# Kernel tuning notes

Hardware: AMD Instinct MI355X
Metric: run time of the kernel (lower is better)

Reference implementation:

```python
import jax, jax.numpy as jnp
import numpy as np

N_NODES = 100000
N_EDGES = 3200000


def _gat_conv(x, src, dst, ea, Wx, We, a_src, a_dst, a_edge, b, n):
    # PyG GATConv, heads=1, edge_dim set: h = x@Wx^T, he = ea@We^T
    h = x @ Wx.T                      # [N,16]
    he = ea @ We.T                    # [E,16]
    alpha = h[src] @ a_src + h[dst] @ a_dst + he @ a_edge  # [E]
    alpha = jnp.where(alpha > 0, alpha, 0.2 * alpha)       # leaky_relu(0.2)
    m = jax.ops.segment_max(alpha, dst, num_segments=n)
    m = jnp.where(jnp.isfinite(m), m, 0.0)
    ex = jnp.exp(alpha - m[dst])
    s = jax.ops.segment_sum(ex, dst, num_segments=n)
    a = ex / (s[dst] + 1e-16)
    out = jax.ops.segment_sum(a[:, None] * h[src], dst, num_segments=n)
    return out + b


def setup_inputs() -> dict:
    key = jax.random.key(0)
    ks = iter(jax.random.split(key, 40))
    rn = lambda shape, s=0.1: jax.random.normal(next(ks), shape, dtype=jnp.float32) * s
    inp = {}
    inp['x'] = jax.random.normal(next(ks), (N_NODES, 4), dtype=jnp.float32)
    inp['edge_index'] = jax.random.randint(next(ks), (2, N_EDGES), 0, N_NODES, dtype=jnp.int64)
    inp['edge_attr'] = jax.random.normal(next(ks), (N_EDGES, 6), dtype=jnp.float32)
    # conv1: GATConv(4->16, edge_dim=6)
    inp['c1_Wx'] = rn((16, 4)); inp['c1_We'] = rn((16, 6))
    inp['c1_asrc'] = rn((16,)); inp['c1_adst'] = rn((16,)); inp['c1_aedge'] = rn((16,))
    inp['c1_b'] = rn((16,))
    # edge1 MLP: 38->32->64->32->16
    inp['e1_w1'] = rn((32, 38)); inp['e1_b1'] = rn((32,))
    inp['e1_w2'] = rn((64, 32)); inp['e1_b2'] = rn((64,))
    inp['e1_w3'] = rn((32, 64)); inp['e1_b3'] = rn((32,))
    inp['e1_w4'] = rn((16, 32)); inp['e1_b4'] = rn((16,))
    # conv2: GATConv(16->16, edge_dim=16)
    inp['c2_Wx'] = rn((16, 16)); inp['c2_We'] = rn((16, 16))
    inp['c2_asrc'] = rn((16,)); inp['c2_adst'] = rn((16,)); inp['c2_aedge'] = rn((16,))
    inp['c2_b'] = rn((16,))
    # node head 16->16->2, edge head 16->16->4
    inp['nl_w1'] = rn((16, 16)); inp['nl_b1'] = rn((16,))
    inp['nl_w2'] = rn((2, 16)); inp['nl_b2'] = rn((2,))
    inp['el_w1'] = rn((16, 16)); inp['el_b1'] = rn((16,))
    inp['el_w2'] = rn((4, 16)); inp['el_b2'] = rn((4,))
    return inp


def reference(x, edge_index, edge_attr,
              c1_Wx, c1_We, c1_asrc, c1_adst, c1_aedge, c1_b,
              e1_w1, e1_b1, e1_w2, e1_b2, e1_w3, e1_b3, e1_w4, e1_b4,
              c2_Wx, c2_We, c2_asrc, c2_adst, c2_aedge, c2_b,
              nl_w1, nl_b1, nl_w2, nl_b2,
              el_w1, el_b1, el_w2, el_b2):
    n = x.shape[0]
    src, dst = edge_index[0], edge_index[1]
    x1 = _gat_conv(x, src, dst, edge_attr, c1_Wx, c1_We, c1_asrc, c1_adst, c1_aedge, c1_b, n)
    # edge MLP on [x_src | edge_attr | x_dst] (dropout = identity in eval)
    e = jnp.concatenate([x1[src], edge_attr, x1[dst]], axis=1)  # [E,38]
    e = jax.nn.relu(e @ e1_w1.T + e1_b1)
    e = jax.nn.relu(e @ e1_w2.T + e1_b2)
    e = jax.nn.relu(e @ e1_w3.T + e1_b3)
    e = e @ e1_w4.T + e1_b4                                     # [E,16]
    x2 = _gat_conv(x1, src, dst, e, c2_Wx, c2_We, c2_asrc, c2_adst, c2_aedge, c2_b, n)
    node = jax.nn.relu(jax.nn.relu(x2 @ nl_w1.T + nl_b1) @ nl_w2.T + nl_b2)
    edge = jax.nn.relu(jax.nn.relu(e @ el_w1.T + el_b1) @ el_w2.T + el_b2)
    return (jax.nn.log_softmax(node, axis=1), jax.nn.log_softmax(edge, axis=1))
```

## Files before the change

kernel.cpp:

```cpp
#include <hip/hip_runtime.h>

#define NN 100000
#define NE 3200000
#define NB 98

typedef unsigned int u32;
typedef unsigned short u16;
typedef _Float16 f16x2 __attribute__((ext_vector_type(2)));
typedef __fp16 fp16v2 __attribute__((ext_vector_type(2)));

__device__ __forceinline__ int clampi(int s){
  s = s < 0 ? 0 : s;
  return s >= NN ? NN-1 : s;
}

__device__ __forceinline__ f16x2 pk2(float x, float y){
  fp16v2 r = __builtin_amdgcn_cvt_pkrtz(x, y);
  return __builtin_bit_cast(f16x2, r);
}
__device__ __forceinline__ float dot2(f16x2 a, f16x2 b, float c){
  return __builtin_amdgcn_fdot2(a, b, c, false);
}
__device__ __forceinline__ float f16lo(u32 w){
  __fp16 h = __builtin_bit_cast(__fp16, (u16)(w & 0xffffu));
  return (float)h;
}
__device__ __forceinline__ float f16hi(u32 w){
  __fp16 h = __builtin_bit_cast(__fp16, (u16)(w >> 16));
  return (float)h;
}
__device__ __forceinline__ float f16u(u16 w){
  __fp16 h = __builtin_bit_cast(__fp16, w);
  return (float)h;
}

__global__ __launch_bounds__(256,8) void khist(const int* __restrict__ ei, int* __restrict__ cnt){
  int i = blockIdx.x*256 + threadIdx.x;
  if (i >= NE) return;
  atomicAdd(&cnt[clampi(ei[NE+i])], 1);
}

__global__ __launch_bounds__(1024) void kscanA(const int* __restrict__ cnt, int* __restrict__ bsum){
  __shared__ int wsum[16];
  int tid = threadIdx.x;
  int i = blockIdx.x*1024 + tid;
  int x = (i < NN) ? cnt[i] : 0;
  #pragma unroll
  for (int ofs = 1; ofs < 64; ofs <<= 1) x += __shfl_xor(x, ofs, 64);
  if ((tid & 63) == 0) wsum[tid >> 6] = x;
  __syncthreads();
  if (tid == 0){
    int t = 0;
    #pragma unroll
    for (int k = 0; k < 16; k++) t += wsum[k];
    bsum[blockIdx.x] = t;
  }
}

__global__ void kscanB(const int* __restrict__ bsum, int* __restrict__ boff, int* __restrict__ offN){
  if (threadIdx.x == 0){
    int c = 0;
    for (int b = 0; b < NB; b++){ boff[b] = c; c += bsum[b]; }
    offN[0] = c;
  }
}

__global__ __launch_bounds__(1024) void kscanC(int* __restrict__ cnt, const int* __restrict__ boff,
                                               int* __restrict__ off){
  __shared__ int wsum[16];
  int tid = threadIdx.x;
  int i = blockIdx.x*1024 + tid;
  int v = (i < NN) ? cnt[i] : 0;
  int x = v;
  #pragma unroll
  for (int ofs = 1; ofs < 64; ofs <<= 1){
    int t = __shfl_up(x, ofs, 64);
    if ((tid & 63) >= ofs) x += t;
  }
  if ((tid & 63) == 63) wsum[tid >> 6] = x;
  __syncthreads();
  if (tid < 16){
    int y = wsum[tid];
    #pragma unroll
    for (int ofs = 1; ofs < 16; ofs <<= 1){
      int t = __shfl_up(y, ofs, 64);
      if (tid >= ofs) y += t;
    }
    wsum[tid] = y;
  }
  __syncthreads();
  int wb = (tid >= 64) ? wsum[(tid >> 6) - 1] : 0;
  if (i < NN){ off[i] = boff[blockIdx.x] + wb + x - v; cnt[i] = 0; }
}

__global__ __launch_bounds__(256,4) void k1(const float* __restrict__ x,
    const float* __restrict__ Wx, const float* __restrict__ asrc, const float* __restrict__ adst,
    float* __restrict__ hs1, float* __restrict__ hd1)
{
  __shared__ float wL[64], aS[16], aD[16];
  int tid = threadIdx.x;
  if (tid < 64) wL[tid] = Wx[tid];
  if (tid < 16){ aS[tid] = asrc[tid]; aD[tid] = adst[tid]; }
  __syncthreads();
  int n = blockIdx.x*256 + tid;
  if (n >= NN) return;
  float4 xr = ((const float4*)x)[n];
  float hs=0.f, hd=0.f;
  #pragma unroll
  for (int j=0;j<16;j++){
    float h = xr.x*wL[j*4+0] + xr.y*wL[j*4+1] + xr.z*wL[j*4+2] + xr.w*wL[j*4+3];
    hs += h*aS[j]; hd += h*aD[j];
  }
  hs1[n]=hs; hd1[n]=hd;
}

__global__ __launch_bounds__(256,8) void k2a(const int* __restrict__ ei,
    const float* __restrict__ ea, const float* __restrict__ We, const float* __restrict__ aedge,
    const float* __restrict__ hs1, const float* __restrict__ hd1,
    const int* __restrict__ off, int* __restrict__ cnt, float2* __restrict__ edata)
{
  __shared__ float w6[6];
  int tid = threadIdx.x;
  if (tid < 6){
    float acc = 0.f;
    for (int j=0;j<16;j++) acc += aedge[j] * We[j*6+tid];
    w6[tid] = acc;
  }
  __syncthreads();
  int i = blockIdx.x*256 + tid;
  if (i >= NE) return;
  int s = clampi(ei[i]);
  int d = clampi(ei[NE + i]);
  const float2* eap = (const float2*)ea + (size_t)i*3;
  float2 u0 = eap[0], u1 = eap[1], u2 = eap[2];
  float al = hs1[s] + hd1[d]
    + u0.x*w6[0] + u0.y*w6[1] + u1.x*w6[2]
    + u1.y*w6[3] + u2.x*w6[4] + u2.y*w6[5];
  al = al > 0.f ? al : 0.2f*al;
  float ex = __expf(al);
  int pos = off[d] + atomicAdd(&cnt[d], 1);
  edata[pos] = make_float2(ex, __int_as_float(s));
}

__global__ __launch_bounds__(256,8) void k34(const float2* __restrict__ edata,
    const int* __restrict__ off, const float* __restrict__ x,
    const float* __restrict__ c1b, const float* __restrict__ Wx1, const float* __restrict__ Wx2,
    const float* __restrict__ a2s, const float* __restrict__ a2d,
    const float* __restrict__ w1p,
    u32* __restrict__ hpk, float* __restrict__ hs2, float* __restrict__ hd2,
    u32* __restrict__ uh, u32* __restrict__ vh, int* __restrict__ cnt)
{
  __shared__ float w0L[64], bL[16], wL[256], aS[16], aD[16];
  __shared__ float w1sL[32*16], w1dL[32*16];
  int tid = threadIdx.x;
  wL[tid] = Wx2[tid];
  if (tid < 64) w0L[tid] = Wx1[tid];
  if (tid < 16){ bL[tid]=c1b[tid]; aS[tid]=a2s[tid]; aD[tid]=a2d[tid]; }
  for (int idx=tid; idx<512; idx+=256){
    int j=idx>>4, k=idx&15;
    w1sL[idx] = w1p[j*38+k];
    w1dL[idx] = w1p[j*38+22+k];
  }
  __syncthreads();
  int t = blockIdx.x*256 + tid;
  int n = t >> 4;
  int j = t & 15;
  if (n >= NN) return;
  int f = j & 3, ks = j >> 2;
  int beg = off[n], end = off[n+1];
  float aj = 0.f, sl = 0.f;
  for (int k = beg + ks; k < end; k += 4){
    float2 p = edata[k];
    int src = __float_as_int(p.y);
    aj += p.x * x[(size_t)src*4 + f];
    sl += p.x;
  }
  aj += __shfl_xor(aj, 4, 64); aj += __shfl_xor(aj, 8, 64);
  sl += __shfl_xor(sl, 4, 64); sl += __shfl_xor(sl, 8, 64);
  float inv = 1.f/(sl + 1e-16f);
  float m0 = __shfl(aj, 0, 16)*inv;
  float m1 = __shfl(aj, 1, 16)*inv;
  float m2 = __shfl(aj, 2, 16)*inv;
  float m3 = __shfl(aj, 3, 16)*inv;
  float xvj = m0*w0L[j*4+0] + m1*w0L[j*4+1] + m2*w0L[j*4+2] + m3*w0L[j*4+3] + bL[j];
  float hv = 0.f, u0=0.f, u1=0.f, v0=0.f, v1=0.f;
  #pragma unroll
  for (int k=0;k<16;k++){
    float vk = __shfl(xvj, k, 16);
    hv += vk * wL[j*16+k];
    u0 += vk * w1sL[(2*j)*16+k];
    u1 += vk * w1sL[(2*j+1)*16+k];
    v0 += vk * w1dL[(2*j)*16+k];
    v1 += vk * w1dL[(2*j+1)*16+k];
  }
  ((u16*)hpk)[(size_t)n*16 + j] = (u16)(__builtin_bit_cast(u32, pk2(hv, 0.f)) & 0xffffu);
  uh[(size_t)n*16 + j] = __builtin_bit_cast(u32, pk2(u0, u1));
  vh[(size_t)n*16 + j] = __builtin_bit_cast(u32, pk2(v0, v1));
  float hsp = hv*aS[j], hdp = hv*aD[j];
  #pragma unroll
  for (int ofs=1; ofs<16; ofs<<=1){
    hsp += __shfl_xor(hsp, ofs, 64);
    hdp += __shfl_xor(hdp, ofs, 64);
  }
  if (j == 0){ hs2[n]=hsp; hd2[n]=hdp; cnt[n]=0; }
}

__global__ __launch_bounds__(256,8) void k5(
    const int* __restrict__ ei, const float* __restrict__ ea,
    const u32* __restrict__ uh, const u32* __restrict__ vh,
    const float* __restrict__ hs2, const float* __restrict__ hd2,
    const float* w1p, const float* b1p, const float* w2p, const float* b2p,
    const float* w3p, const float* b3p, const float* w4p, const float* b4p,
    const float* We2, const float* a2e,
    const float* ew1p, const float* eb1p, const float* ew2p, const float* eb2p,
    const int* __restrict__ off, int* __restrict__ cnt, float2* __restrict__ edata,
    float* __restrict__ eout)
{
  __shared__ __align__(16) f16x2 w1eh[32*4];  __shared__ float b1L[32];
  __shared__ __align__(16) f16x2 w2h[64*16];  __shared__ float b2L[64];
  __shared__ __align__(16) f16x2 w3h[32*32];  __shared__ float b3L[32];
  __shared__ __align__(16) f16x2 w4h[16*16];  __shared__ float b4L[16];
  __shared__ __align__(16) f16x2 ew1h[16*8];  __shared__ float eb1L[16];
  __shared__ __align__(16) f16x2 ew2h[4*8];   __shared__ float eb2L[4];
  __shared__ __align__(16) f16x2 w16h[8];
  int tid = threadIdx.x;
  if (tid < 128){
    int j=tid>>2, kk=tid&3;
    int k0=2*kk, k1=2*kk+1;
    float v0 = (k0<6) ? w1p[j*38+16+k0] : 0.f;
    float v1 = (k1<6) ? w1p[j*38+16+k1] : 0.f;
    w1eh[tid] = pk2(v0, v1);
  }
  for (int idx=tid; idx<1024; idx+=256){
    int j=idx>>4, kk=idx&15;
    w2h[idx] = pk2(w2p[j*32+2*kk], w2p[j*32+2*kk+1]);
  }
  for (int idx=tid; idx<1024; idx+=256){
    int j=idx>>5, kk=idx&31;
    w3h[idx] = pk2(w3p[j*64+2*kk], w3p[j*64+2*kk+1]);
  }
  if (tid < 256){
    int j=tid>>4, kk=tid&15;
    w4h[tid] = pk2(w4p[j*32+2*kk], w4p[j*32+2*kk+1]);
  }
  if (tid < 128){
    int j=tid>>3, kk=tid&7;
    ew1h[tid] = pk2(ew1p[j*16+2*kk], ew1p[j*16+2*kk+1]);
  }
  if (tid < 32){
    int j=tid>>3, kk=tid&7;
    ew2h[tid] = pk2(ew2p[j*16+2*kk], ew2p[j*16+2*kk+1]);
  }
  if (tid < 8){
    float s0=0.f, s1=0.f;
    for (int j=0;j<16;j++){
      s0 += a2e[j] * We2[j*16 + 2*tid];
      s1 += a2e[j] * We2[j*16 + 2*tid + 1];
    }
    w16h[tid] = pk2(s0, s1);
  }
  if (tid < 64) b2L[tid] = b2p[tid];
  if (tid < 32){ b1L[tid] = b1p[tid]; b3L[tid] = b3p[tid]; }
  if (tid < 16){ b4L[tid] = b4p[tid]; eb1L[tid] = eb1p[tid]; }
  if (tid < 4)  eb2L[tid] = eb2p[tid];
  __syncthreads();

  int i = blockIdx.x*256 + tid;
  if (i >= NE) return;
  int s = clampi(ei[i]);
  int d = clampi(ei[NE + i]);

  f16x2 a1h[16];
  {
    const float2* eap = (const float2*)ea + (size_t)i*3;
    float2 e0=eap[0], e1=eap[1], e2=eap[2];
    f16x2 eh[4];
    eh[0]=pk2(e0.x,e0.y); eh[1]=pk2(e1.x,e1.y); eh[2]=pk2(e2.x,e2.y); eh[3]=pk2(0.f,0.f);
    const uint4* up = (const uint4*)(uh + (size_t)s*16);
    const uint4* vp = (const uint4*)(vh + (size_t)d*16);
    uint4 U[4], V[4];
    #pragma unroll
    for (int q=0;q<4;q++){ U[q]=up[q]; V[q]=vp[q]; }
    u32 uw[16], vw[16];
    #pragma unroll
    for (int q=0;q<4;q++){
      uw[4*q]=U[q].x; uw[4*q+1]=U[q].y; uw[4*q+2]=U[q].z; uw[4*q+3]=U[q].w;
      vw[4*q]=V[q].x; vw[4*q+1]=V[q].y; vw[4*q+2]=V[q].z; vw[4*q+3]=V[q].w;
    }
    #pragma unroll
    for (int j=0;j<16;j++){
      float t0 = b1L[2*j]   + f16lo(uw[j]) + f16lo(vw[j]);
      float t1 = b1L[2*j+1] + f16hi(uw[j]) + f16hi(vw[j]);
      #pragma unroll
      for (int kk=0;kk<4;kk++){
        t0 = dot2(eh[kk], w1eh[(2*j)*4+kk],   t0);
        t1 = dot2(eh[kk], w1eh[(2*j+1)*4+kk], t1);
      }
      a1h[j] = pk2(fmaxf(t0,0.f), fmaxf(t1,0.f));
    }
  }
  f16x2 a2h[32];
  #pragma unroll
  for (int j=0;j<32;j++){
    float acc0 = b2L[2*j], acc1 = b2L[2*j+1];
    #pragma unroll
    for (int kk=0;kk<16;kk++){
      acc0 = dot2(a1h[kk], w2h[(2*j)*16+kk],   acc0);
      acc1 = dot2(a1h[kk], w2h[(2*j+1)*16+kk], acc1);
    }
    a2h[j] = pk2(fmaxf(acc0,0.f), fmaxf(acc1,0.f));
  }
  f16x2 a3h[16];
  #pragma unroll
  for (int j=0;j<16;j++){
    float acc0 = b3L[2*j], acc1 = b3L[2*j+1];
    #pragma unroll
    for (int kk=0;kk<32;kk++){
      acc0 = dot2(a2h[kk], w3h[(2*j)*32+kk],   acc0);
      acc1 = dot2(a2h[kk], w3h[(2*j+1)*32+kk], acc1);
    }
    a3h[j] = pk2(fmaxf(acc0,0.f), fmaxf(acc1,0.f));
  }
  f16x2 eh4[8];
  #pragma unroll
  for (int j=0;j<8;j++){
    float acc0 = b4L[2*j], acc1 = b4L[2*j+1];
    #pragma unroll
    for (int kk=0;kk<16;kk++){
      acc0 = dot2(a3h[kk], w4h[(2*j)*16+kk],   acc0);
      acc1 = dot2(a3h[kk], w4h[(2*j+1)*16+kk], acc1);
    }
    eh4[j] = pk2(acc0, acc1);
  }
  f16x2 th[8];
  #pragma unroll
  for (int j=0;j<8;j++){
    float acc0 = eb1L[2*j], acc1 = eb1L[2*j+1];
    #pragma unroll
    for (int kk=0;kk<8;kk++){
      acc0 = dot2(eh4[kk], ew1h[(2*j)*8+kk],   acc0);
      acc1 = dot2(eh4[kk], ew1h[(2*j+1)*8+kk], acc1);
    }
    th[j] = pk2(fmaxf(acc0,0.f), fmaxf(acc1,0.f));
  }
  float y0 = eb2L[0], y1 = eb2L[1], y2 = eb2L[2], y3 = eb2L[3];
  #pragma unroll
  for (int kk=0;kk<8;kk++){
    y0 = dot2(th[kk], ew2h[0*8+kk], y0);
    y1 = dot2(th[kk], ew2h[1*8+kk], y1);
    y2 = dot2(th[kk], ew2h[2*8+kk], y2);
    y3 = dot2(th[kk], ew2h[3*8+kk], y3);
  }
  y0 = fmaxf(y0,0.f); y1 = fmaxf(y1,0.f); y2 = fmaxf(y2,0.f); y3 = fmaxf(y3,0.f);
  float m = fmaxf(fmaxf(y0,y1), fmaxf(y2,y3));
  float l = m + __logf(__expf(y0-m)+__expf(y1-m)+__expf(y2-m)+__expf(y3-m));
  float4 eo; eo.x = y0-l; eo.y = y1-l; eo.z = y2-l; eo.w = y3-l;
  ((float4*)eout)[i] = eo;

  float al = hs2[s] + hd2[d];
  #pragma unroll
  for (int kk=0;kk<8;kk++) al = dot2(eh4[kk], w16h[kk], al);
  al = al > 0.f ? al : 0.2f*al;
  float ex = __expf(al);
  int pos = off[d] + atomicAdd(&cnt[d], 1);
  edata[pos] = make_float2(ex, __int_as_float(s));
}

__global__ __launch_bounds__(256,8) void kagg2(const float2* __restrict__ edata,
    const int* __restrict__ off, const u16* __restrict__ hpk,
    const float* __restrict__ c2b,
    const float* __restrict__ w1p, const float* __restrict__ b1p,
    const float* __restrict__ w2p, const float* __restrict__ b2p,
    float* __restrict__ nout, int* __restrict__ cnt)
{
  __shared__ float w1L[256], cb[16], b1L[16], w2L[32], b2L[2];
  int tid = threadIdx.x;
  w1L[tid] = w1p[tid];
  if (tid < 16){ cb[tid] = c2b[tid]; b1L[tid] = b1p[tid]; }
  if (tid < 32) w2L[tid] = w2p[tid];
  if (tid < 2)  b2L[tid] = b2p[tid];
  __syncthreads();
  int t = blockIdx.x*256 + tid;
  int n = t >> 6;
  int l = t & 63;
  if (n >= NN) return;
  int j = l & 15, ks = l >> 4;
  int beg = off[n], end = off[n+1];
  float aj = 0.f, sl = 0.f;
  for (int k = beg + ks; k < end; k += 4){
    float2 p = edata[k];
    int src = __float_as_int(p.y);
    aj += p.x * f16u(hpk[(size_t)src*16 + j]);
    sl += p.x;
  }
  aj += __shfl_xor(aj, 16, 64); aj += __shfl_xor(aj, 32, 64);
  sl += __shfl_xor(sl, 16, 64); sl += __shfl_xor(sl, 32, 64);
  float inv = 1.f/(sl + 1e-16f);
  float vj = aj*inv + cb[j];
  float tj = b1L[j];
  #pragma unroll
  for (int k=0;k<16;k++){
    float vk = __shfl(vj, k, 16);
    tj += vk * w1L[j*16 + k];
  }
  tj = fmaxf(tj, 0.f);
  float p0 = tj * w2L[j];
  float p1 = tj * w2L[16 + j];
  #pragma unroll
  for (int ofs=1; ofs<16; ofs<<=1){
    p0 += __shfl_xor(p0, ofs, 64);
    p1 += __shfl_xor(p1, ofs, 64);
  }
  if (l == 0){
    float y0 = fmaxf(p0 + b2L[0], 0.f);
    float y1 = fmaxf(p1 + b2L[1], 0.f);
    float m = fmaxf(y0, y1);
    float lg = m + __logf(__expf(y0-m) + __expf(y1-m));
    float2 no; no.x = y0-lg; no.y = y1-lg;
    ((float2*)nout)[n] = no;
    cnt[n] = 0;
  }
}

extern "C" void kernel_launch(void* const* d_in, const int* in_sizes, int n_in,
                              void* d_out, int out_size, void* d_ws, size_t ws_size,
                              hipStream_t stream)
{
  const float* x  = (const float*)d_in[0];
  const int* ei   = (const int*)d_in[1];
  const float* ea = (const float*)d_in[2];
  const float* c1Wx = (const float*)d_in[3];
  const float* c1We = (const float*)d_in[4];
  const float* c1as = (const float*)d_in[5];
  const float* c1ad = (const float*)d_in[6];
  const float* c1ae = (const float*)d_in[7];
  const float* c1b  = (const float*)d_in[8];
  const float* e1w1 = (const float*)d_in[9];
  const float* e1b1 = (const float*)d_in[10];
  const float* e1w2 = (const float*)d_in[11];
  const float* e1b2 = (const float*)d_in[12];
  const float* e1w3 = (const float*)d_in[13];
  const float* e1b3 = (const float*)d_in[14];
  const float* e1w4 = (const float*)d_in[15];
  const float* e1b4 = (const float*)d_in[16];
  const float* c2Wx = (const float*)d_in[17];
  const float* c2We = (const float*)d_in[18];
  const float* c2as = (const float*)d_in[19];
  const float* c2ad = (const float*)d_in[20];
  const float* c2ae = (const float*)d_in[21];
  const float* c2b  = (const float*)d_in[22];
  const float* nlw1 = (const float*)d_in[23];
  const float* nlb1 = (const float*)d_in[24];
  const float* nlw2 = (const float*)d_in[25];
  const float* nlb2 = (const float*)d_in[26];
  const float* elw1 = (const float*)d_in[27];
  const float* elb1 = (const float*)d_in[28];
  const float* elw2 = (const float*)d_in[29];
  const float* elb2 = (const float*)d_in[30];

  float* ws = (float*)d_ws;
  const size_t N = NN;
  int* off   = (int*)ws;
  int* cnt   = (int*)ws + (N + 8);
  int* bsum  = (int*)ws + (2*N + 8);
  int* boff  = (int*)ws + (2*N + 136);
  u32* hpk   = (u32*)(ws + 2*N + 264);
  float* hs  = ws + 10*N + 264;
  float* hd  = hs + N;
  u32* uh    = (u32*)(hd + N);
  u32* vh    = uh + 16*N;
  float2* edata = (float2*)(vh + 16*N);

  float* nout = (float*)d_out;
  float* eout = (float*)d_out + 200000;

  const int GE = (NE + 255)/256;
  const int GN = (NN + 255)/256;

  (void)hipMemsetAsync(cnt, 0, N*sizeof(int), stream);
  khist<<<GE, 256, 0, stream>>>(ei, cnt);
  kscanA<<<NB, 1024, 0, stream>>>(cnt, bsum);
  kscanB<<<1, 64, 0, stream>>>(bsum, boff, off + NN);
  kscanC<<<NB, 1024, 0, stream>>>(cnt, boff, off);
  k1<<<GN, 256, 0, stream>>>(x, c1Wx, c1as, c1ad, hs, hd);
  k2a<<<GE, 256, 0, stream>>>(ei, ea, c1We, c1ae, hs, hd, off, cnt, edata);
  k34<<<(NN*16 + 255)/256, 256, 0, stream>>>(edata, off, x,
      c1b, c1Wx, c2Wx, c2as, c2ad, e1w1, hpk, hs, hd, uh, vh, cnt);
  k5<<<GE, 256, 0, stream>>>(ei, ea, uh, vh, hs, hd,
      e1w1, e1b1, e1w2, e1b2, e1w3, e1b3, e1w4, e1b4,
      c2We, c2ae, elw1, elb1, elw2, elb2,
      off, cnt, edata, eout);
  kagg2<<<(NN*64 + 255)/256, 256, 0, stream>>>(edata, off, (const u16*)hpk,
      c2b, nlw1, nlb1, nlw2, nlb2, nout, cnt);
}
```

Before: 766.7 us.

## Run edge MLP layers 2-3 on MFMA and fold layer 4 into downstream weights

The per-edge MLP's 32->64 and 64->32 layers move from per-thread fdot2 loops to 16x16x32 f16 MFMA instructions. Each wave stages its activations through shared memory in 16-row tiles. The linear fourth layer is folded algebraically into the edge-head first layer and into the attention-edge vector, which removes a matmul per edge. The costs are extra LDS traffic, many block-wide barriers inside the tile loop, and lower occupancy from launch bounds 4 and larger shared memory. The NE bounds check is dropped, which is safe only because NE is a multiple of 256.

```diff
diff --git a/kernel.cpp b/kernel.cpp
--- a/kernel.cpp
+++ b/kernel.cpp
@@ -7,6 +7,8 @@
 typedef unsigned int u32;
 typedef unsigned short u16;
 typedef _Float16 f16x2 __attribute__((ext_vector_type(2)));
+typedef _Float16 f16x8 __attribute__((ext_vector_type(8)));
+typedef float fltx4 __attribute__((ext_vector_type(4)));
 typedef __fp16 fp16v2 __attribute__((ext_vector_type(2)));
 
 __device__ __forceinline__ int clampi(int s){
@@ -17,6 +19,9 @@
 __device__ __forceinline__ f16x2 pk2(float x, float y){
   fp16v2 r = __builtin_amdgcn_cvt_pkrtz(x, y);
   return __builtin_bit_cast(f16x2, r);
+}
+__device__ __forceinline__ u32 pk2u(float x, float y){
+  return __builtin_bit_cast(u32, pk2(x, y));
 }
 __device__ __forceinline__ float dot2(f16x2 a, f16x2 b, float c){
   return __builtin_amdgcn_fdot2(a, b, c, false);
@@ -193,9 +198,9 @@
     v0 += vk * w1dL[(2*j)*16+k];
     v1 += vk * w1dL[(2*j+1)*16+k];
   }
-  ((u16*)hpk)[(size_t)n*16 + j] = (u16)(__builtin_bit_cast(u32, pk2(hv, 0.f)) & 0xffffu);
-  uh[(size_t)n*16 + j] = __builtin_bit_cast(u32, pk2(u0, u1));
-  vh[(size_t)n*16 + j] = __builtin_bit_cast(u32, pk2(v0, v1));
+  ((u16*)hpk)[(size_t)n*16 + j] = (u16)(pk2u(hv, 0.f) & 0xffffu);
+  uh[(size_t)n*16 + j] = pk2u(u0, u1);
+  vh[(size_t)n*16 + j] = pk2u(v0, v1);
   float hsp = hv*aS[j], hdp = hv*aD[j];
   #pragma unroll
   for (int ofs=1; ofs<16; ofs<<=1){
@@ -205,7 +210,7 @@
   if (j == 0){ hs2[n]=hsp; hd2[n]=hdp; cnt[n]=0; }
 }
 
-__global__ __launch_bounds__(256,8) void k5(
+__global__ __launch_bounds__(256,4) void k5m(
     const int* __restrict__ ei, const float* __restrict__ ea,
     const u32* __restrict__ uh, const u32* __restrict__ vh,
     const float* __restrict__ hs2, const float* __restrict__ hd2,
@@ -216,13 +221,17 @@
     const int* __restrict__ off, int* __restrict__ cnt, float2* __restrict__ edata,
     float* __restrict__ eout)
 {
+  __shared__ __align__(16) u32 a13L[4][1024];
+  __shared__ __align__(16) u32 a2L[4][512];
+  __shared__ __align__(16) uint4 b2f[4][64];
+  __shared__ __align__(16) uint4 b3f[4][64];
   __shared__ __align__(16) f16x2 w1eh[32*4];  __shared__ float b1L[32];
-  __shared__ __align__(16) f16x2 w2h[64*16];  __shared__ float b2L[64];
-  __shared__ __align__(16) f16x2 w3h[32*32];  __shared__ float b3L[32];
-  __shared__ __align__(16) f16x2 w4h[16*16];  __shared__ float b4L[16];
-  __shared__ __align__(16) f16x2 ew1h[16*8];  __shared__ float eb1L[16];
+  __shared__ float b2L[64], b3L[32];
+  __shared__ __align__(16) f16x2 M1h[16*16];  __shared__ float c1L[16];
   __shared__ __align__(16) f16x2 ew2h[4*8];   __shared__ float eb2L[4];
-  __shared__ __align__(16) f16x2 w16h[8];
+  __shared__ __align__(16) f16x2 w16w4h[16];
+  __shared__ float w16L[16];  __shared__ float w16b4L;
+
   int tid = threadIdx.x;
   if (tid < 128){
     int j=tid>>2, kk=tid&3;
@@ -231,46 +240,75 @@
     float v1 = (k1<6) ? w1p[j*38+16+k1] : 0.f;
     w1eh[tid] = pk2(v0, v1);
   }
-  for (int idx=tid; idx<1024; idx+=256){
-    int j=idx>>4, kk=idx&15;
-    w2h[idx] = pk2(w2p[j*32+2*kk], w2p[j*32+2*kk+1]);
-  }
-  for (int idx=tid; idx<1024; idx+=256){
-    int j=idx>>5, kk=idx&31;
-    w3h[idx] = pk2(w3p[j*64+2*kk], w3p[j*64+2*kk+1]);
-  }
-  if (tid < 256){
-    int j=tid>>4, kk=tid&15;
-    w4h[tid] = pk2(w4p[j*32+2*kk], w4p[j*32+2*kk+1]);
-  }
-  if (tid < 128){
-    int j=tid>>3, kk=tid&7;
-    ew1h[tid] = pk2(ew1p[j*16+2*kk], ew1p[j*16+2*kk+1]);
+  {
+    int c = tid>>6, l = tid&63;
+    int j = c*16 + (l&15), kb = (l>>4)*8;
+    const float* src = w2p + j*32 + kb;
+    uint4 q;
+    q.x = pk2u(src[0], src[1]); q.y = pk2u(src[2], src[3]);
+    q.z = pk2u(src[4], src[5]); q.w = pk2u(src[6], src[7]);
+    b2f[c][l] = q;
+  }
+  {
+    int kt = tid>>7, c = (tid>>6)&1, l = tid&63;
+    int j = c*16 + (l&15), kb = kt*32 + (l>>4)*8;
+    const float* src = w3p + j*64 + kb;
+    uint4 q;
+    q.x = pk2u(src[0], src[1]); q.y = pk2u(src[2], src[3]);
+    q.z = pk2u(src[4], src[5]); q.w = pk2u(src[6], src[7]);
+    b3f[kt*2+c][l] = q;
+  }
+  if (tid < 64) b2L[tid] = b2p[tid];
+  if (tid < 32){ b1L[tid] = b1p[tid]; b3L[tid] = b3p[tid]; }
+  {
+    int o = tid>>4, p = tid&15;
+    float m0=0.f, m1=0.f;
+    #pragma unroll
+    for (int q=0;q<16;q++){
+      float w = ew1p[o*16+q];
+      m0 += w * w4p[q*32 + 2*p];
+      m1 += w * w4p[q*32 + 2*p + 1];
+    }
+    M1h[o*16+p] = pk2(m0, m1);
+  }
+  if (tid < 16){
+    float acc = eb1p[tid];
+    for (int q=0;q<16;q++) acc += ew1p[tid*16+q]*b4p[q];
+    c1L[tid] = acc;
+    float w=0.f;
+    for (int j=0;j<16;j++) w += a2e[j] * We2[j*16+tid];
+    w16L[tid] = w;
   }
   if (tid < 32){
     int j=tid>>3, kk=tid&7;
     ew2h[tid] = pk2(ew2p[j*16+2*kk], ew2p[j*16+2*kk+1]);
   }
-  if (tid < 8){
+  if (tid < 4) eb2L[tid] = eb2p[tid];
+  __syncthreads();
+  if (tid < 16){
     float s0=0.f, s1=0.f;
-    for (int j=0;j<16;j++){
-      s0 += a2e[j] * We2[j*16 + 2*tid];
-      s1 += a2e[j] * We2[j*16 + 2*tid + 1];
-    }
-    w16h[tid] = pk2(s0, s1);
-  }
-  if (tid < 64) b2L[tid] = b2p[tid];
-  if (tid < 32){ b1L[tid] = b1p[tid]; b3L[tid] = b3p[tid]; }
-  if (tid < 16){ b4L[tid] = b4p[tid]; eb1L[tid] = eb1p[tid]; }
-  if (tid < 4)  eb2L[tid] = eb2p[tid];
-  __syncthreads();
-
+    for (int q=0;q<16;q++){
+      s0 += w16L[q]*w4p[q*32 + 2*tid];
+      s1 += w16L[q]*w4p[q*32 + 2*tid + 1];
+    }
+    w16w4h[tid] = pk2(s0, s1);
+  }
+  if (tid == 0){
+    float acc=0.f;
+    for (int q=0;q<16;q++) acc += w16L[q]*b4p[q];
+    w16b4L = acc;
+  }
+  __syncthreads();
+
+  int wid = tid>>6, lane = tid&63;
+  int cl = lane & 15, g = lane >> 4;
+  u32* a13 = a13L[wid];
+  u32* a2u = a2L[wid];
   int i = blockIdx.x*256 + tid;
-  if (i >= NE) return;
   int s = clampi(ei[i]);
   int d = clampi(ei[NE + i]);
 
-  f16x2 a1h[16];
+  u32 a1h[16];
   {
     const float2* eap = (const float2*)ea + (size_t)i*3;
     float2 e0=eap[0], e1=eap[1], e2=eap[2];
@@ -296,52 +334,82 @@
         t0 = dot2(eh[kk], w1eh[(2*j)*4+kk],   t0);
         t1 = dot2(eh[kk], w1eh[(2*j+1)*4+kk], t1);
       }
-      a1h[j] = pk2(fmaxf(t0,0.f), fmaxf(t1,0.f));
-    }
-  }
-  f16x2 a2h[32];
-  #pragma unroll
-  for (int j=0;j<32;j++){
-    float acc0 = b2L[2*j], acc1 = b2L[2*j+1];
-    #pragma unroll
-    for (int kk=0;kk<16;kk++){
-      acc0 = dot2(a1h[kk], w2h[(2*j)*16+kk],   acc0);
-      acc1 = dot2(a1h[kk], w2h[(2*j+1)*16+kk], acc1);
-    }
-    a2h[j] = pk2(fmaxf(acc0,0.f), fmaxf(acc1,0.f));
-  }
-  f16x2 a3h[16];
-  #pragma unroll
-  for (int j=0;j<16;j++){
-    float acc0 = b3L[2*j], acc1 = b3L[2*j+1];
-    #pragma unroll
-    for (int kk=0;kk<32;kk++){
-      acc0 = dot2(a2h[kk], w3h[(2*j)*32+kk],   acc0);
-      acc1 = dot2(a2h[kk], w3h[(2*j+1)*32+kk], acc1);
-    }
-    a3h[j] = pk2(fmaxf(acc0,0.f), fmaxf(acc1,0.f));
-  }
-  f16x2 eh4[8];
-  #pragma unroll
-  for (int j=0;j<8;j++){
-    float acc0 = b4L[2*j], acc1 = b4L[2*j+1];
-    #pragma unroll
-    for (int kk=0;kk<16;kk++){
-      acc0 = dot2(a3h[kk], w4h[(2*j)*16+kk],   acc0);
-      acc1 = dot2(a3h[kk], w4h[(2*j+1)*16+kk], acc1);
-    }
-    eh4[j] = pk2(acc0, acc1);
+      a1h[j] = pk2u(fmaxf(t0,0.f), fmaxf(t1,0.f));
+    }
+  }
+  {
+    uint4* dst = (uint4*)(a13 + lane*16);
+    dst[0] = make_uint4(a1h[0],a1h[1],a1h[2],a1h[3]);
+    dst[1] = make_uint4(a1h[4],a1h[5],a1h[6],a1h[7]);
+    dst[2] = make_uint4(a1h[8],a1h[9],a1h[10],a1h[11]);
+    dst[3] = make_uint4(a1h[12],a1h[13],a1h[14],a1h[15]);
+  }
+  f16x8 fb2[4], fb3[4];
+  #pragma unroll
+  for (int c=0;c<4;c++) fb2[c] = __builtin_bit_cast(f16x8, b2f[c][lane]);
+  #pragma unroll
+  for (int q=0;q<4;q++) fb3[q] = __builtin_bit_cast(f16x8, b3f[q][lane]);
+  __syncthreads();
+
+  #pragma unroll
+  for (int r=0;r<4;r++){
+    __syncthreads();
+    uint4 av = *(const uint4*)(a13 + (r*16 + cl)*16 + g*4);
+    f16x8 af = __builtin_bit_cast(f16x8, av);
+    _Float16* a2h_ = (_Float16*)a2u;
+    #pragma unroll
+    for (int c=0;c<4;c++){
+      float b = b2L[c*16 + cl];
+      fltx4 acc = {b,b,b,b};
+      acc = __builtin_amdgcn_mfma_f32_16x16x32_f16(af, fb2[c], acc, 0, 0, 0);
+      int col = c*16 + cl;
+      int rowb = g*4;
+      a2h_[(rowb+0)*64 + col] = (_Float16)fmaxf(acc[0], 0.f);
+      a2h_[(rowb+1)*64 + col] = (_Float16)fmaxf(acc[1], 0.f);
+      a2h_[(rowb+2)*64 + col] = (_Float16)fmaxf(acc[2], 0.f);
+      a2h_[(rowb+3)*64 + col] = (_Float16)fmaxf(acc[3], 0.f);
+    }
+    __syncthreads();
+    uint4 a20 = *(const uint4*)(a2u + cl*32 + g*4);
+    uint4 a21 = *(const uint4*)(a2u + cl*32 + 16 + g*4);
+    f16x8 af0 = __builtin_bit_cast(f16x8, a20);
+    f16x8 af1 = __builtin_bit_cast(f16x8, a21);
+    _Float16* a3w = (_Float16*)a13;
+    #pragma unroll
+    for (int c=0;c<2;c++){
+      float b = b3L[c*16 + cl];
+      fltx4 acc = {b,b,b,b};
+      acc = __builtin_amdgcn_mfma_f32_16x16x32_f16(af0, fb3[0*2+c], acc, 0, 0, 0);
+      acc = __builtin_amdgcn_mfma_f32_16x16x32_f16(af1, fb3[1*2+c], acc, 0, 0, 0);
+      int col = c*16 + cl;
+      int row = r*16 + g*4;
+      a3w[(row+0)*32 + col] = (_Float16)fmaxf(acc[0], 0.f);
+      a3w[(row+1)*32 + col] = (_Float16)fmaxf(acc[1], 0.f);
+      a3w[(row+2)*32 + col] = (_Float16)fmaxf(acc[2], 0.f);
+      a3w[(row+3)*32 + col] = (_Float16)fmaxf(acc[3], 0.f);
+    }
+  }
+  __syncthreads();
+  u32 a3h[16];
+  {
+    const uint4* srcp = (const uint4*)(a13 + lane*16);
+    uint4 q0=srcp[0], q1=srcp[1], q2=srcp[2], q3=srcp[3];
+    a3h[0]=q0.x; a3h[1]=q0.y; a3h[2]=q0.z; a3h[3]=q0.w;
+    a3h[4]=q1.x; a3h[5]=q1.y; a3h[6]=q1.z; a3h[7]=q1.w;
+    a3h[8]=q2.x; a3h[9]=q2.y; a3h[10]=q2.z; a3h[11]=q2.w;
+    a3h[12]=q3.x; a3h[13]=q3.y; a3h[14]=q3.z; a3h[15]=q3.w;
   }
   f16x2 th[8];
   #pragma unroll
-  for (int j=0;j<8;j++){
-    float acc0 = eb1L[2*j], acc1 = eb1L[2*j+1];
-    #pragma unroll
-    for (int kk=0;kk<8;kk++){
-      acc0 = dot2(eh4[kk], ew1h[(2*j)*8+kk],   acc0);
-      acc1 = dot2(eh4[kk], ew1h[(2*j+1)*8+kk], acc1);
-    }
-    th[j] = pk2(fmaxf(acc0,0.f), fmaxf(acc1,0.f));
+  for (int o=0;o<8;o++){
+    float t0 = c1L[2*o], t1 = c1L[2*o+1];
+    #pragma unroll
+    for (int kp=0;kp<16;kp++){
+      f16x2 a = __builtin_bit_cast(f16x2, a3h[kp]);
+      t0 = dot2(a, M1h[(2*o)*16+kp],   t0);
+      t1 = dot2(a, M1h[(2*o+1)*16+kp], t1);
+    }
+    th[o] = pk2(fmaxf(t0,0.f), fmaxf(t1,0.f));
   }
   float y0 = eb2L[0], y1 = eb2L[1], y2 = eb2L[2], y3 = eb2L[3];
   #pragma unroll
@@ -357,9 +425,12 @@
   float4 eo; eo.x = y0-l; eo.y = y1-l; eo.z = y2-l; eo.w = y3-l;
   ((float4*)eout)[i] = eo;
 
-  float al = hs2[s] + hd2[d];
-  #pragma unroll
-  for (int kk=0;kk<8;kk++) al = dot2(eh4[kk], w16h[kk], al);
+  float al = hs2[s] + hd2[d] + w16b4L;
+  #pragma unroll
+  for (int kp=0;kp<16;kp++){
+    f16x2 a = __builtin_bit_cast(f16x2, a3h[kp]);
+    al = dot2(a, w16w4h[kp], al);
+  }
   al = al > 0.f ? al : 0.2f*al;
   float ex = __expf(al);
   int pos = off[d] + atomicAdd(&cnt[d], 1);
@@ -486,7 +557,7 @@
   k2a<<<GE, 256, 0, stream>>>(ei, ea, c1We, c1ae, hs, hd, off, cnt, edata);
   k34<<<(NN*16 + 255)/256, 256, 0, stream>>>(edata, off, x,
       c1b, c1Wx, c2Wx, c2as, c2ad, e1w1, hpk, hs, hd, uh, vh, cnt);
-  k5<<<GE, 256, 0, stream>>>(ei, ea, uh, vh, hs, hd,
+  k5m<<<GE, 256, 0, stream>>>(ei, ea, uh, vh, hs, hd,
       e1w1, e1b1, e1w2, e1b2, e1w3, e1b3, e1w4, e1b4,
       c2We, c2ae, elw1, elb1, elw2, elb2,
       off, cnt, edata, eout);
```

After: 742.3 us. -3.2%, faster.
